# Kernel tuning notes

Measured on AMD Instinct MI355X. Metric: run time of the kernel, lower is better.

Reference implementation:

```python
import jax, jax.numpy as jnp
import numpy as np

VOCAB, EMB, HID, OUT_VOCAB, LAYERS = 256, 512, 1024, 256, 2
B, T = 128, 512
LN_EPS = 1e-5


def _run_layer(seq_tbi, Wi, bi, Wh):
    # seq_tbi: [T, B, in_dim]; Wi: [H, in_dim]; bi: [H]; Wh: [H, H]
    h0 = jnp.zeros((seq_tbi.shape[1], Wh.shape[0]), dtype=seq_tbi.dtype)
    xproj = jnp.einsum('tbi,hi->tbh', seq_tbi, Wi) + bi  # precompute input projection

    def step(h, xp_t):
        h_new = jnp.tanh(xp_t + h @ Wh.T)
        return h_new, h_new

    _, hs = jax.lax.scan(step, h0, xproj)  # hs: [T, B, H]
    return hs


def setup_inputs() -> dict:
    key = jax.random.key(0)
    ks = jax.random.split(key, 10)

    def xavier(k, shape):
        fan_in, fan_out = shape[1], shape[0]
        lim = np.sqrt(6.0 / (fan_in + fan_out))
        return jax.random.uniform(k, shape, jnp.float32, -lim, lim)

    def ortho(k, n):
        a = jax.random.normal(k, (n, n), jnp.float32)
        q, r = jnp.linalg.qr(a)
        return q * jnp.sign(jnp.diag(r))[None, :]

    emb = xavier(ks[0], (VOCAB, EMB))
    wi0 = xavier(ks[1], (HID, EMB))
    bi0 = jnp.zeros((HID,), jnp.float32)
    wh0 = ortho(ks[2], HID)
    wi1 = xavier(ks[3], (HID, HID))
    bi1 = jnp.zeros((HID,), jnp.float32)
    wh1 = ortho(ks[4], HID)
    ln_g = jnp.ones((HID,), jnp.float32)
    ln_b = jnp.zeros((HID,), jnp.float32)
    proj_w = xavier(ks[5], (OUT_VOCAB, HID))
    proj_b = jnp.zeros((OUT_VOCAB,), jnp.float32)
    x = jax.random.randint(ks[6], (B, T), 0, VOCAB)
    return {"emb": emb, "wi0": wi0, "bi0": bi0, "wh0": wh0,
            "wi1": wi1, "bi1": bi1, "wh1": wh1,
            "ln_g": ln_g, "ln_b": ln_b, "proj_w": proj_w, "proj_b": proj_b,
            "x": x}


def reference(emb, wi0, bi0, wh0, wi1, bi1, wh1, ln_g, ln_b, proj_w, proj_b, x):
    # x: [B, T] int -> embeddings [T, B, E] (time-major for scan)
    embs = emb[x].transpose(1, 0, 2)
    hs = _run_layer(embs, wi0, bi0, wh0)      # [T, B, H]
    hs = _run_layer(hs, wi1, bi1, wh1)        # [T, B, H]
    # LayerNorm over last dim, then projection, vectorized over all steps
    mu = hs.mean(-1, keepdims=True)
    var = ((hs - mu) ** 2).mean(-1, keepdims=True)
    normed = (hs - mu) * jax.lax.rsqrt(var + LN_EPS) * ln_g + ln_b
    logits = jnp.einsum('tbh,vh->tbv', normed, proj_w) + proj_b
    return logits.transpose(1, 0, 2)  # [B, T, OUT_VOCAB]
```

## Files before the change

### kernel.cpp

```cpp
#include <hip/hip_runtime.h>
#include <hip/hip_bf16.h>


typedef __bf16 bf16;
typedef _Float16 f16;
typedef _Float16 f16x8 __attribute__((ext_vector_type(8)));
typedef float f32x4 __attribute__((ext_vector_type(4)));
typedef unsigned long long u64;

#define TSTEPS 512
#define BATCH  128
#define HID    1024
#define NST    515

__device__ __forceinline__ f32x4 mfma16(f16x8 a, f16x8 b, f32x4 c) {
    return __builtin_amdgcn_mfma_f32_16x16x32_f16(a, b, c, 0, 0, 0);
}

__device__ __forceinline__ f16x8 lda16(const f16* p) {
    union { u64 u[2]; f16x8 v; } c;
    c.u[0] = __hip_atomic_load((const u64*)p,     __ATOMIC_RELAXED, __HIP_MEMORY_SCOPE_AGENT);
    c.u[1] = __hip_atomic_load((const u64*)p + 1, __ATOMIC_RELAXED, __HIP_MEMORY_SCOPE_AGENT);
    return c.v;
}
__device__ __forceinline__ void sth2(f16* p, f16 v) {
    union { f16 f; unsigned short s; } c; c.f = v;
    __hip_atomic_store((unsigned short*)p, c.s, __ATOMIC_RELAXED, __HIP_MEMORY_SCOPE_AGENT);
}
__device__ __forceinline__ void stf4(float* p, float v) {
    union { float f; unsigned u; } c; c.f = v;
    __hip_atomic_store((unsigned*)p, c.u, __ATOMIC_RELAXED, __HIP_MEMORY_SCOPE_AGENT);
}
__device__ __forceinline__ float ldf4c(const float* p) {
    union { float f; unsigned u; } c;
    c.u = __hip_atomic_load((const unsigned*)p, __ATOMIC_RELAXED, __HIP_MEMORY_SCOPE_AGENT);
    return c.f;
}

__device__ __forceinline__ float ldf(const void* p, size_t i, bool f32) {
    return f32 ? ((const float*)p)[i] : (float)((const bf16*)p)[i];
}

__global__ void det_kernel(const unsigned short* __restrict__ e, unsigned* __restrict__ flag) {
    int tid = threadIdx.x;
    int cnt = 0;
    for (int i = tid; i < 1024; i += 256) {
        unsigned short u = e[i];
        int ex = (u >> 7) & 0xFF;
        if ((ex >= 110 && ex <= 131) || u == 0) cnt++;
    }
    __shared__ int sh[256];
    sh[tid] = cnt; __syncthreads();
    for (int s = 128; s > 0; s >>= 1) { if (tid < s) sh[tid] += sh[tid + s]; __syncthreads(); }
    if (tid == 0) *flag = (sh[0] >= 768) ? 0u : 1u;
}

__global__ void etab_kernel(const void* __restrict__ emb, const void* __restrict__ wi0,
                            const void* __restrict__ bi0, const unsigned* __restrict__ flag,
                            float* __restrict__ etab) {
    const bool f32 = (*flag != 0);
    int i = blockIdx.x * 256 + threadIdx.x;
    int v = i >> 10, ch = i & 1023;
    float s = ldf(bi0, ch, f32);
    for (int e = 0; e < 512; ++e)
        s += ldf(emb, (size_t)v * 512 + e, f32) * ldf(wi0, (size_t)ch * 512 + e, f32);
    etab[i] = s;
}

__global__ void c12_kernel(const void* __restrict__ pw, const void* __restrict__ g,
                           const void* __restrict__ be, const void* __restrict__ pb,
                           const unsigned* __restrict__ flag, float* __restrict__ c12) {
    const bool f32 = (*flag != 0);
    int v = threadIdx.x;
    float a = 0.f, b = 0.f;
    for (int k = 0; k < 1024; ++k) {
        float w = ldf(pw, (size_t)v * 1024 + k, f32);
        a += (float)(f16)(w * ldf(g, k, f32));
        b += w * ldf(be, k, f32);
    }
    c12[v] = a;
    c12[256 + v] = b + ldf(pb, v, f32);
}

__global__ __launch_bounds__(512, 2) void mega_kernel(
    const void* __restrict__ wh0, const void* __restrict__ wi1,
    const void* __restrict__ wh1, const void* __restrict__ pw,
    const void* __restrict__ lng, const void* __restrict__ bi1,
    const float* __restrict__ etab, const float* __restrict__ c12,
    const int* __restrict__ x, const unsigned* __restrict__ flag,
    f16* __restrict__ h0buf, f16* __restrict__ h1buf, float* __restrict__ xpf,
    void* __restrict__ out, unsigned* __restrict__ cnt)
{
    const bool f32io = (*flag != 0);
    const int bid  = blockIdx.x;
    const int g    = bid & 7, rid = bid >> 3;
    const int role = rid >> 3;
    const int slice = rid & 7;
    const int tid  = threadIdx.x;
    const int wave = tid >> 6, lane = tid & 63;
    const int n    = lane & 15, quad = lane >> 4;
    const int gbase = g * 16;
    unsigned* const myc = cnt + g * 32;

    __shared__ f16 As[16][1032];

    f16x8 wf[32];
    float bias = 0.f, c1v = 0.f, c2v = 0.f;
    int ch = 0, outv = 0;
    if (role < 3) {
        ch = slice * 128 + wave * 16 + n;
        const void* W = (role == 0) ? wh0 : ((role == 1) ? wi1 : wh1);
#pragma unroll
        for (int kt = 0; kt < 32; ++kt) {
            f16x8 t;
#pragma unroll
            for (int j = 0; j < 8; ++j)
                t[j] = (f16)ldf(W, (size_t)ch * HID + kt * 32 + quad * 8 + j, f32io);
            wf[kt] = t;
        }
        if (role == 1) bias = ldf(bi1, ch, f32io);
    } else {
        int tile = slice * 8 + wave;
        outv = tile * 16 + n;
#pragma unroll
        for (int kt = 0; kt < 32; ++kt) {
            f16x8 t;
#pragma unroll
            for (int j = 0; j < 8; ++j) {
                int k = kt * 32 + quad * 8 + j;
                t[j] = (f16)(ldf(pw, (size_t)outv * HID + k, f32io) * ldf(lng, k, f32io));
            }
            wf[kt] = t;
        }
        c1v = c12[outv];
        c2v = c12[256 + outv];
    }

    for (int t = 0; t < NST; ++t) {
        bool active;
        f16* rbuf;
        if (role == 0)      { active = (t < 512);            rbuf = h0buf; }
        else if (role == 1) { active = (t >= 1 && t <= 512); rbuf = h0buf; }
        else if (role == 2) { active = (t >= 2 && t <= 513); rbuf = h1buf; }
        else                { active = (t >= 3 && t <= 514); rbuf = h1buf; }

        if (active) {
            const f16* Abase = rbuf + ((t + 1) & 1) * (BATCH * HID)
                             + (size_t)gbase * HID;
#pragma unroll
            for (int it = 0; it < 4; ++it) {
                int idx = it * 512 + tid;
                int row = idx >> 7, col = (idx & 127) << 3;
                f16x8 v = lda16(Abase + (size_t)row * HID + col);
                *(f16x8*)&As[row][col] = v;
            }

            float ev[4] = {0.f, 0.f, 0.f, 0.f};
            if (role == 0) {
#pragma unroll
                for (int r = 0; r < 4; ++r) {
                    int b = gbase + quad * 4 + r;
                    ev[r] = etab[(size_t)x[b * TSTEPS + t] * HID + ch];
                }
            } else if (role == 2) {
                const float* xs = xpf + (t & 1) * (BATCH * HID);
#pragma unroll
                for (int r = 0; r < 4; ++r)
                    ev[r] = ldf4c(xs + (size_t)(gbase + quad * 4 + r) * HID + ch);
            }

            __syncthreads();

            float mu = 0.f, rs = 0.f;
            if (role == 3) {
                const f16* srow = &As[n][quad * 256];
                float sum = 0.f, sq = 0.f;
#pragma unroll
                for (int i = 0; i < 256; i += 8) {
                    f16x8 hv = *(const f16x8*)(srow + i);
#pragma unroll
                    for (int j = 0; j < 8; ++j) {
                        float e = (float)hv[j];
                        sum += e; sq += e * e;
                    }
                }
                sum += __shfl_xor(sum, 16); sq += __shfl_xor(sq, 16);
                sum += __shfl_xor(sum, 32); sq += __shfl_xor(sq, 32);
                mu = sum * (1.f / 1024.f);
                float var = sq * (1.f / 1024.f) - mu * mu;
                rs = rsqrtf(fmaxf(var, 0.f) + 1e-5f);
            }

            const f16* arow = &As[n][quad * 8];
            f32x4 a0 = {0,0,0,0}, a1 = {0,0,0,0}, a2 = {0,0,0,0}, a3 = {0,0,0,0};
#pragma unroll
            for (int kt = 0; kt < 32; kt += 4) {
                a0 = mfma16(*(const f16x8*)(arow + (kt + 0) * 32), wf[kt + 0], a0);
                a1 = mfma16(*(const f16x8*)(arow + (kt + 1) * 32), wf[kt + 1], a1);
                a2 = mfma16(*(const f16x8*)(arow + (kt + 2) * 32), wf[kt + 2], a2);
                a3 = mfma16(*(const f16x8*)(arow + (kt + 3) * 32), wf[kt + 3], a3);
            }
            f32x4 acc = (a0 + a1) + (a2 + a3);

            if (role == 0) {
                f16* dw = h0buf + (t & 1) * (BATCH * HID);
#pragma unroll
                for (int r = 0; r < 4; ++r) {
                    int b = gbase + quad * 4 + r;
                    sth2(dw + (size_t)b * HID + ch, (f16)tanhf(acc[r] + ev[r]));
                }
            } else if (role == 1) {
                float* dw = xpf + ((t + 1) & 1) * (BATCH * HID);
#pragma unroll
                for (int r = 0; r < 4; ++r) {
                    int b = gbase + quad * 4 + r;
                    stf4(dw + (size_t)b * HID + ch, acc[r] + bias);
                }
            } else if (role == 2) {
                f16* dw = h1buf + (t & 1) * (BATCH * HID);
#pragma unroll
                for (int r = 0; r < 4; ++r) {
                    int b = gbase + quad * 4 + r;
                    sth2(dw + (size_t)b * HID + ch, (f16)tanhf(acc[r] + ev[r]));
                }
            } else {
                int s = t - 3;
#pragma unroll
                for (int r = 0; r < 4; ++r) {
                    int m = quad * 4 + r;
                    float mm = __shfl(mu, m), rr = __shfl(rs, m);
                    float lv = rr * acc[r] - rr * mm * c1v + c2v;
                    size_t oi = ((size_t)(gbase + m) * TSTEPS + s) * 256 + outv;
                    if (f32io) ((float*)out)[oi] = lv;
                    else       ((bf16*)out)[oi]  = (bf16)lv;
                }
            }
        }

        __syncthreads();
        if (tid == 0) {
            __hip_atomic_fetch_add(myc, 1u, __ATOMIC_RELAXED, __HIP_MEMORY_SCOPE_AGENT);
            const unsigned tgt = 26u * (unsigned)(t + 1);
            while (__hip_atomic_load(myc, __ATOMIC_RELAXED, __HIP_MEMORY_SCOPE_AGENT) < tgt)
                __builtin_amdgcn_s_sleep(1);
        }
        __syncthreads();
    }
}

extern "C" void kernel_launch(void* const* d_in, const int* in_sizes, int n_in,
                              void* d_out, int out_size, void* d_ws, size_t ws_size,
                              hipStream_t stream) {
    const void* emb    = d_in[0];
    const void* wi0    = d_in[1];
    const void* bi0    = d_in[2];
    const void* wh0    = d_in[3];
    const void* wi1    = d_in[4];
    const void* bi1    = d_in[5];
    const void* wh1    = d_in[6];
    const void* ln_g   = d_in[7];
    const void* ln_b   = d_in[8];
    const void* proj_w = d_in[9];
    const void* proj_b = d_in[10];
    const int*  x      = (const int*)d_in[11];
    char* ws = (char*)d_ws;

    float*    etab  = (float*)(ws + 0);
    float*    c12   = (float*)(ws + 1048576);
    unsigned* flag  = (unsigned*)(ws + 1050624);
    f16*      h0buf = (f16*)(ws + 1050688);
    f16*      h1buf = (f16*)(ws + 1574976);
    float*    xpf   = (float*)(ws + 2099264);
    unsigned* cnt   = (unsigned*)(ws + 3147840);
    if (ws_size < 3151936u) return;

    hipMemsetAsync(ws + 1050624, 0, 3151936 - 1050624, stream);

    det_kernel<<<1, 256, 0, stream>>>((const unsigned short*)emb, flag);
    etab_kernel<<<1024, 256, 0, stream>>>(emb, wi0, bi0, flag, etab);
    c12_kernel<<<1, 256, 0, stream>>>(proj_w, ln_g, ln_b, proj_b, flag, c12);
    mega_kernel<<<208, 512, 0, stream>>>(wh0, wi1, wh1, proj_w, ln_g, bi1,
                                         etab, c12, x, flag,
                                         h0buf, h1buf, xpf, d_out, cnt);
}
```

Before: 3.835 ms.

## Use XCC-local cache coherence path when a whole group shares one XCD

At startup each block records its XCC id, and each group of 26 cooperating blocks checks whether all its members landed on the same XCD. If they did, the recurrent loop uses inline-asm loads and stores with only the sc0 bit, so they stay coherent in the shared per-XCD L2 instead of going through device-scope atomics. Otherwise it falls back to the original agent-scope atomic path. The change relies on the hardware's block placement and on MI300-family cache semantics, and correctness depends on the detection being right.

```diff
diff --git a/kernel.cpp b/kernel.cpp
--- a/kernel.cpp
+++ b/kernel.cpp
@@ -35,6 +35,10 @@
     union { float f; unsigned u; } c;
     c.u = __hip_atomic_load((const unsigned*)p, __ATOMIC_RELAXED, __HIP_MEMORY_SCOPE_AGENT);
     return c.f;
+}
+
+__device__ __forceinline__ unsigned f16bits32(f16 v) {
+    union { f16 f; unsigned short s; } c; c.f = v; return (unsigned)c.s;
 }
 
 __device__ __forceinline__ float ldf(const void* p, size_t i, bool f32) {
@@ -80,6 +84,203 @@
     }
     c12[v] = a;
     c12[256 + v] = b + ldf(pb, v, f32);
+}
+
+template<bool FAST>
+__device__ __forceinline__ void run_loop(
+    const int role, const int gbase,
+    const int tid, const int lane, const int n, const int quad,
+    const int ch, const int outv,
+    const f16x8 (&wf)[32], const float bias, const float c1v, const float c2v,
+    const bool f32io,
+    const float* __restrict__ etab, const int* __restrict__ x,
+    f16* __restrict__ h0buf, f16* __restrict__ h1buf, float* __restrict__ xpf,
+    void* __restrict__ out, unsigned* __restrict__ myc,
+    f16 (&As)[16][1032])
+{
+    for (int t = 0; t < NST; ++t) {
+        bool active;
+        f16* rbuf;
+        if (role == 0)      { active = (t < 512);            rbuf = h0buf; }
+        else if (role == 1) { active = (t >= 1 && t <= 512); rbuf = h0buf; }
+        else if (role == 2) { active = (t >= 2 && t <= 513); rbuf = h1buf; }
+        else                { active = (t >= 3 && t <= 514); rbuf = h1buf; }
+
+        if (active) {
+            const f16* Abase = rbuf + ((t + 1) & 1) * (BATCH * HID)
+                             + (size_t)gbase * HID;
+
+            float ev[4] = {0.f, 0.f, 0.f, 0.f};
+            if (role == 0) {
+#pragma unroll
+                for (int r = 0; r < 4; ++r) {
+                    int b = gbase + quad * 4 + r;
+                    ev[r] = etab[(size_t)x[b * TSTEPS + t] * HID + ch];
+                }
+            } else if (role == 2) {
+                const float* xs = xpf + (t & 1) * (BATCH * HID);
+                if constexpr (FAST) {
+                    const float* p0 = xs + (size_t)(gbase + quad * 4 + 0) * HID + ch;
+                    const float* p1 = xs + (size_t)(gbase + quad * 4 + 1) * HID + ch;
+                    const float* p2 = xs + (size_t)(gbase + quad * 4 + 2) * HID + ch;
+                    const float* p3 = xs + (size_t)(gbase + quad * 4 + 3) * HID + ch;
+                    asm volatile(
+                        "global_load_dword %0, %4, off sc0\n\t"
+                        "global_load_dword %1, %5, off sc0\n\t"
+                        "global_load_dword %2, %6, off sc0\n\t"
+                        "global_load_dword %3, %7, off sc0\n\t"
+                        "s_waitcnt vmcnt(0)"
+                        : "=&v"(ev[0]), "=&v"(ev[1]), "=&v"(ev[2]), "=&v"(ev[3])
+                        : "v"(p0), "v"(p1), "v"(p2), "v"(p3)
+                        : "memory");
+                } else {
+#pragma unroll
+                    for (int r = 0; r < 4; ++r)
+                        ev[r] = ldf4c(xs + (size_t)(gbase + quad * 4 + r) * HID + ch);
+                }
+            }
+
+            if constexpr (FAST) {
+                const f16* ga[4]; f16* da[4];
+#pragma unroll
+                for (int it = 0; it < 4; ++it) {
+                    int idx = it * 512 + tid;
+                    int row = idx >> 7, col = (idx & 127) << 3;
+                    ga[it] = Abase + (size_t)row * HID + col;
+                    da[it] = &As[row][col];
+                }
+                f32x4 v0, v1, v2, v3;
+                asm volatile(
+                    "global_load_dwordx4 %0, %4, off sc0\n\t"
+                    "global_load_dwordx4 %1, %5, off sc0\n\t"
+                    "global_load_dwordx4 %2, %6, off sc0\n\t"
+                    "global_load_dwordx4 %3, %7, off sc0\n\t"
+                    "s_waitcnt vmcnt(0)"
+                    : "=&v"(v0), "=&v"(v1), "=&v"(v2), "=&v"(v3)
+                    : "v"(ga[0]), "v"(ga[1]), "v"(ga[2]), "v"(ga[3])
+                    : "memory");
+                *(f32x4*)da[0] = v0;
+                *(f32x4*)da[1] = v1;
+                *(f32x4*)da[2] = v2;
+                *(f32x4*)da[3] = v3;
+            } else {
+#pragma unroll
+                for (int it = 0; it < 4; ++it) {
+                    int idx = it * 512 + tid;
+                    int row = idx >> 7, col = (idx & 127) << 3;
+                    f16x8 v = lda16(Abase + (size_t)row * HID + col);
+                    *(f16x8*)&As[row][col] = v;
+                }
+            }
+
+            __syncthreads();
+
+            float mu = 0.f, rs = 0.f;
+            if (role == 3) {
+                const f16* srow = &As[n][quad * 256];
+                float sum = 0.f, sq = 0.f;
+#pragma unroll
+                for (int i = 0; i < 256; i += 8) {
+                    f16x8 hv = *(const f16x8*)(srow + i);
+#pragma unroll
+                    for (int j = 0; j < 8; ++j) {
+                        float e = (float)hv[j];
+                        sum += e; sq += e * e;
+                    }
+                }
+                sum += __shfl_xor(sum, 16); sq += __shfl_xor(sq, 16);
+                sum += __shfl_xor(sum, 32); sq += __shfl_xor(sq, 32);
+                mu = sum * (1.f / 1024.f);
+                float var = sq * (1.f / 1024.f) - mu * mu;
+                rs = rsqrtf(fmaxf(var, 0.f) + 1e-5f);
+            }
+
+            const f16* arow = &As[n][quad * 8];
+            f32x4 a0 = {0,0,0,0}, a1 = {0,0,0,0}, a2 = {0,0,0,0}, a3 = {0,0,0,0};
+#pragma unroll
+            for (int kt = 0; kt < 32; kt += 4) {
+                a0 = mfma16(*(const f16x8*)(arow + (kt + 0) * 32), wf[kt + 0], a0);
+                a1 = mfma16(*(const f16x8*)(arow + (kt + 1) * 32), wf[kt + 1], a1);
+                a2 = mfma16(*(const f16x8*)(arow + (kt + 2) * 32), wf[kt + 2], a2);
+                a3 = mfma16(*(const f16x8*)(arow + (kt + 3) * 32), wf[kt + 3], a3);
+            }
+            f32x4 acc = (a0 + a1) + (a2 + a3);
+
+            if (role == 0 || role == 2) {
+                f16* dw = ((role == 0) ? h0buf : h1buf) + (t & 1) * (BATCH * HID);
+                if constexpr (FAST) {
+                    unsigned u0 = f16bits32((f16)tanhf(acc[0] + ev[0]));
+                    unsigned u1 = f16bits32((f16)tanhf(acc[1] + ev[1]));
+                    unsigned u2 = f16bits32((f16)tanhf(acc[2] + ev[2]));
+                    unsigned u3 = f16bits32((f16)tanhf(acc[3] + ev[3]));
+                    f16* q0 = dw + (size_t)(gbase + quad * 4 + 0) * HID + ch;
+                    f16* q1 = dw + (size_t)(gbase + quad * 4 + 1) * HID + ch;
+                    f16* q2 = dw + (size_t)(gbase + quad * 4 + 2) * HID + ch;
+                    f16* q3 = dw + (size_t)(gbase + quad * 4 + 3) * HID + ch;
+                    asm volatile(
+                        "global_store_short %4, %0, off sc0\n\t"
+                        "global_store_short %5, %1, off sc0\n\t"
+                        "global_store_short %6, %2, off sc0\n\t"
+                        "global_store_short %7, %3, off sc0\n\t"
+                        "s_waitcnt vmcnt(0)"
+                        :: "v"(u0), "v"(u1), "v"(u2), "v"(u3),
+                           "v"(q0), "v"(q1), "v"(q2), "v"(q3)
+                        : "memory");
+                } else {
+#pragma unroll
+                    for (int r = 0; r < 4; ++r) {
+                        int b = gbase + quad * 4 + r;
+                        sth2(dw + (size_t)b * HID + ch, (f16)tanhf(acc[r] + ev[r]));
+                    }
+                }
+            } else if (role == 1) {
+                float* dw = xpf + ((t + 1) & 1) * (BATCH * HID);
+                if constexpr (FAST) {
+                    float w0 = acc[0] + bias, w1 = acc[1] + bias;
+                    float w2 = acc[2] + bias, w3 = acc[3] + bias;
+                    float* q0 = dw + (size_t)(gbase + quad * 4 + 0) * HID + ch;
+                    float* q1 = dw + (size_t)(gbase + quad * 4 + 1) * HID + ch;
+                    float* q2 = dw + (size_t)(gbase + quad * 4 + 2) * HID + ch;
+                    float* q3 = dw + (size_t)(gbase + quad * 4 + 3) * HID + ch;
+                    asm volatile(
+                        "global_store_dword %4, %0, off sc0\n\t"
+                        "global_store_dword %5, %1, off sc0\n\t"
+                        "global_store_dword %6, %2, off sc0\n\t"
+                        "global_store_dword %7, %3, off sc0\n\t"
+                        "s_waitcnt vmcnt(0)"
+                        :: "v"(w0), "v"(w1), "v"(w2), "v"(w3),
+                           "v"(q0), "v"(q1), "v"(q2), "v"(q3)
+                        : "memory");
+                } else {
+#pragma unroll
+                    for (int r = 0; r < 4; ++r) {
+                        int b = gbase + quad * 4 + r;
+                        stf4(dw + (size_t)b * HID + ch, acc[r] + bias);
+                    }
+                }
+            } else {
+                int s = t - 3;
+#pragma unroll
+                for (int r = 0; r < 4; ++r) {
+                    int m = quad * 4 + r;
+                    float mm = __shfl(mu, m), rr = __shfl(rs, m);
+                    float lv = rr * acc[r] - rr * mm * c1v + c2v;
+                    size_t oi = ((size_t)(gbase + m) * TSTEPS + s) * 256 + outv;
+                    if (f32io) ((float*)out)[oi] = lv;
+                    else       ((bf16*)out)[oi]  = (bf16)lv;
+                }
+            }
+        }
+
+        __syncthreads();
+        if (tid == 0) {
+            __hip_atomic_fetch_add(myc, 1u, __ATOMIC_RELAXED, __HIP_MEMORY_SCOPE_AGENT);
+            const unsigned tgt = 26u * (unsigned)(t + 1);
+            while (__hip_atomic_load(myc, __ATOMIC_RELAXED, __HIP_MEMORY_SCOPE_AGENT) < tgt)
+                __builtin_amdgcn_s_sleep(1);
+        }
+        __syncthreads();
+    }
 }
 
 __global__ __launch_bounds__(512, 2) void mega_kernel(
@@ -102,7 +303,7 @@
     const int gbase = g * 16;
     unsigned* const myc = cnt + g * 32;
 
-    __shared__ f16 As[16][1032];
+    __shared__ __align__(16) f16 As[16][1032];
 
     f16x8 wf[32];
     float bias = 0.f, c1v = 0.f, c2v = 0.f;
@@ -136,116 +337,34 @@
         c2v = c12[256 + outv];
     }
 
-    for (int t = 0; t < NST; ++t) {
-        bool active;
-        f16* rbuf;
-        if (role == 0)      { active = (t < 512);            rbuf = h0buf; }
-        else if (role == 1) { active = (t >= 1 && t <= 512); rbuf = h0buf; }
-        else if (role == 2) { active = (t >= 2 && t <= 513); rbuf = h1buf; }
-        else                { active = (t >= 3 && t <= 514); rbuf = h1buf; }
-
-        if (active) {
-            const f16* Abase = rbuf + ((t + 1) & 1) * (BATCH * HID)
-                             + (size_t)gbase * HID;
-#pragma unroll
-            for (int it = 0; it < 4; ++it) {
-                int idx = it * 512 + tid;
-                int row = idx >> 7, col = (idx & 127) << 3;
-                f16x8 v = lda16(Abase + (size_t)row * HID + col);
-                *(f16x8*)&As[row][col] = v;
-            }
-
-            float ev[4] = {0.f, 0.f, 0.f, 0.f};
-            if (role == 0) {
-#pragma unroll
-                for (int r = 0; r < 4; ++r) {
-                    int b = gbase + quad * 4 + r;
-                    ev[r] = etab[(size_t)x[b * TSTEPS + t] * HID + ch];
-                }
-            } else if (role == 2) {
-                const float* xs = xpf + (t & 1) * (BATCH * HID);
-#pragma unroll
-                for (int r = 0; r < 4; ++r)
-                    ev[r] = ldf4c(xs + (size_t)(gbase + quad * 4 + r) * HID + ch);
-            }
-
-            __syncthreads();
-
-            float mu = 0.f, rs = 0.f;
-            if (role == 3) {
-                const f16* srow = &As[n][quad * 256];
-                float sum = 0.f, sq = 0.f;
-#pragma unroll
-                for (int i = 0; i < 256; i += 8) {
-                    f16x8 hv = *(const f16x8*)(srow + i);
-#pragma unroll
-                    for (int j = 0; j < 8; ++j) {
-                        float e = (float)hv[j];
-                        sum += e; sq += e * e;
-                    }
-                }
-                sum += __shfl_xor(sum, 16); sq += __shfl_xor(sq, 16);
-                sum += __shfl_xor(sum, 32); sq += __shfl_xor(sq, 32);
-                mu = sum * (1.f / 1024.f);
-                float var = sq * (1.f / 1024.f) - mu * mu;
-                rs = rsqrtf(fmaxf(var, 0.f) + 1e-5f);
-            }
-
-            const f16* arow = &As[n][quad * 8];
-            f32x4 a0 = {0,0,0,0}, a1 = {0,0,0,0}, a2 = {0,0,0,0}, a3 = {0,0,0,0};
-#pragma unroll
-            for (int kt = 0; kt < 32; kt += 4) {
-                a0 = mfma16(*(const f16x8*)(arow + (kt + 0) * 32), wf[kt + 0], a0);
-                a1 = mfma16(*(const f16x8*)(arow + (kt + 1) * 32), wf[kt + 1], a1);
-                a2 = mfma16(*(const f16x8*)(arow + (kt + 2) * 32), wf[kt + 2], a2);
-                a3 = mfma16(*(const f16x8*)(arow + (kt + 3) * 32), wf[kt + 3], a3);
-            }
-            f32x4 acc = (a0 + a1) + (a2 + a3);
-
-            if (role == 0) {
-                f16* dw = h0buf + (t & 1) * (BATCH * HID);
-#pragma unroll
-                for (int r = 0; r < 4; ++r) {
-                    int b = gbase + quad * 4 + r;
-                    sth2(dw + (size_t)b * HID + ch, (f16)tanhf(acc[r] + ev[r]));
-                }
-            } else if (role == 1) {
-                float* dw = xpf + ((t + 1) & 1) * (BATCH * HID);
-#pragma unroll
-                for (int r = 0; r < 4; ++r) {
-                    int b = gbase + quad * 4 + r;
-                    stf4(dw + (size_t)b * HID + ch, acc[r] + bias);
-                }
-            } else if (role == 2) {
-                f16* dw = h1buf + (t & 1) * (BATCH * HID);
-#pragma unroll
-                for (int r = 0; r < 4; ++r) {
-                    int b = gbase + quad * 4 + r;
-                    sth2(dw + (size_t)b * HID + ch, (f16)tanhf(acc[r] + ev[r]));
-                }
-            } else {
-                int s = t - 3;
-#pragma unroll
-                for (int r = 0; r < 4; ++r) {
-                    int m = quad * 4 + r;
-                    float mm = __shfl(mu, m), rr = __shfl(rs, m);
-                    float lv = rr * acc[r] - rr * mm * c1v + c2v;
-                    size_t oi = ((size_t)(gbase + m) * TSTEPS + s) * 256 + outv;
-                    if (f32io) ((float*)out)[oi] = lv;
-                    else       ((bf16*)out)[oi]  = (bf16)lv;
-                }
-            }
+    unsigned xcc = 0;
+    asm volatile("s_getreg_b32 %0, hwreg(HW_REG_XCC_ID)" : "=s"(xcc));
+    xcc &= 0xFu;
+    __shared__ int fsh;
+    if (tid == 0) {
+        const unsigned my = 0x100u | xcc;
+        __hip_atomic_store(cnt + 256 + bid, my, __ATOMIC_RELAXED, __HIP_MEMORY_SCOPE_AGENT);
+        int ok = 1;
+        for (int r = 0; r < 26; ++r) {
+            unsigned v;
+            for (;;) {
+                v = __hip_atomic_load(cnt + 256 + g + 8 * r, __ATOMIC_RELAXED, __HIP_MEMORY_SCOPE_AGENT);
+                if (v & 0x100u) break;
+                __builtin_amdgcn_s_sleep(2);
+            }
+            if (v != my) ok = 0;
         }
-
-        __syncthreads();
-        if (tid == 0) {
-            __hip_atomic_fetch_add(myc, 1u, __ATOMIC_RELAXED, __HIP_MEMORY_SCOPE_AGENT);
-            const unsigned tgt = 26u * (unsigned)(t + 1);
-            while (__hip_atomic_load(myc, __ATOMIC_RELAXED, __HIP_MEMORY_SCOPE_AGENT) < tgt)
-                __builtin_amdgcn_s_sleep(1);
-        }
-        __syncthreads();
+        fsh = ok;
     }
+    __syncthreads();
+    const bool fast = (fsh != 0);
+
+    if (fast)
+        run_loop<true >(role, gbase, tid, lane, n, quad, ch, outv, wf, bias, c1v, c2v,
+                        f32io, etab, x, h0buf, h1buf, xpf, out, myc, As);
+    else
+        run_loop<false>(role, gbase, tid, lane, n, quad, ch, outv, wf, bias, c1v, c2v,
+                        f32io, etab, x, h0buf, h1buf, xpf, out, myc, As);
 }
 
 extern "C" void kernel_launch(void* const* d_in, const int* in_sizes, int n_in,
```

Measured after the change: 3.446 ms. 10.2% less time.
